# Kernel optimization log

Measured on AMD Instinct MI355X. Metric: run time of the kernel, lower is better.

Reference implementation:

```python
import jax, jax.numpy as jnp
import numpy as np

B, T, C = 4, 4096, 1024


def setup_inputs() -> dict:
    key = jax.random.key(0)
    k_x, k_f, k_g, k_p = jax.random.split(key, 4)
    scale = 1.0 / np.sqrt(C)  # keep gate pre-activations well-scaled
    return {
        "x": jax.random.normal(k_x, (B, T, C), dtype=jnp.float32),
        "W_f_x": jax.random.normal(k_f, (C, C), dtype=jnp.float32) * scale,
        "W_g_x": jax.random.normal(k_g, (C, C), dtype=jnp.float32) * scale,
        "W_proj": jax.random.normal(k_p, (C, C), dtype=jnp.float32) * scale,
    }


def _cfc_scan(a, b):
    """Solve h_t = a_t * h_{t-1} + b_t with h_{-1}=0 along axis 1 (T).

    Associative op on linear maps: (A_l,B_l) then (A_r,B_r) composes to
    (A_r*A_l, A_r*B_l + B_r). With h_init=0, h_t = B-component.
    """
    def op(l, r):
        al, bl = l
        ar, br = r
        return ar * al, ar * bl + br
    _, h = jax.lax.associative_scan(op, (a, b), axis=1)
    return h


def reference(x, W_f_x, W_g_x, W_proj):
    # Gates depend on x only (parallel mode). nn.Linear: x @ W.T
    f = jax.nn.sigmoid(jnp.einsum("btc,dc->btd", x, W_f_x))  # (B,T,C)
    g = jnp.tanh(jnp.einsum("btc,dc->btd", x, W_g_x))        # (B,T,C)
    h = _cfc_scan(f, (1.0 - f) * g)                           # (B,T,C)
    return jnp.einsum("btc,dc->btd", h, W_proj)               # c_proj
```

## Files before the change

kernel.cpp:

```cpp
#include <hip/hip_runtime.h>
#include <hip/hip_bf16.h>
#include <stdint.h>

#define TT 4096
#define BB 4
#define CC 1024
#define MM (BB * TT)
#define NCHUNK 64
#define CHUNK_T (TT / NCHUNK)
#define NCHAIN (BB * CC)

typedef float f32x4 __attribute__((ext_vector_type(4)));
typedef __bf16 bf16x8 __attribute__((ext_vector_type(8)));
typedef ushort us8 __attribute__((ext_vector_type(8)));

__device__ __forceinline__ float b2f(ushort u) {
  union { float f; uint32_t v; } x; x.v = ((uint32_t)u) << 16; return x.f;
}
__device__ __forceinline__ ushort f2b(float f) {
  union { float f; uint32_t u; } x; x.f = f;
  uint32_t r = x.u + 0x7fffu + ((x.u >> 16) & 1u);
  return (ushort)(r >> 16);
}

__device__ __forceinline__ void async_copy16(const ushort* g, ushort* l) {
  __builtin_amdgcn_global_load_lds(
      (__attribute__((address_space(1))) void*)(g),
      (__attribute__((address_space(3))) void*)(l), 16, 0, 0);
}

__global__ __launch_bounds__(256) void cvt_all(const float* __restrict__ x,
                                               const float* __restrict__ wf,
                                               const float* __restrict__ wg,
                                               const float* __restrict__ wp,
                                               ushort* __restrict__ xb,
                                               ushort* __restrict__ wcat,
                                               ushort* __restrict__ wpb) {
  const int i = blockIdx.x * 256 + threadIdx.x;
  const float* s; ushort* d; int off, dst;
  if (i < 4194304) {
    s = x; d = xb; off = i; dst = i;
  } else if (i < 4456448) {
    s = wf; d = wcat; off = i - 4194304;
    dst = ((off >> 8) << 9) + (off & 255);
  } else if (i < 4718592) {
    s = wg; d = wcat; off = i - 4456448;
    dst = ((off >> 8) << 9) + 256 + (off & 255);
  } else {
    s = wp; d = wpb; off = i - 4718592; dst = off;
  }
  float4 v = ((const float4*)s)[off];
  ushort4 o;
  o.x = f2b(v.x); o.y = f2b(v.y); o.z = f2b(v.z); o.w = f2b(v.w);
  ((ushort4*)d)[dst] = o;
}


#define RDA(sl, ih)                                                       \
  _Pragma("unroll") for (int i_ = 0; i_ < 4; ++i_)                        \
      af[i_] = *(const bf16x8*)(rA + (sl) * 8192 + (ih) * 2048 + i_ * 512);

#define RDB(sl)                                                           \
  _Pragma("unroll") for (int j_ = 0; j_ < 4; ++j_)                        \
      bfr[j_] = *(const bf16x8*)(rB + (sl) * 8192 + j_ * 512);

#define MFMA16(ih)                                                        \
  __builtin_amdgcn_s_setprio(1);                                          \
  _Pragma("unroll") for (int i_ = 0; i_ < 4; ++i_)                        \
  _Pragma("unroll") for (int j_ = 0; j_ < 4; ++j_)                        \
      acc[(ih) * 4 + i_][j_] = __builtin_amdgcn_mfma_f32_16x16x32_bf16(   \
          bfr[j_], af[i_], acc[(ih) * 4 + i_][j_], 0, 0, 0);              \
  __builtin_amdgcn_s_setprio(0)

#define MIDBAR()                                                          \
  __builtin_amdgcn_s_barrier();                                           \
  asm volatile("s_waitcnt lgkmcnt(0)" ::: "memory");                      \
  __builtin_amdgcn_sched_barrier(0)

#define ENDBAR()                                                          \
  __builtin_amdgcn_s_barrier();                                           \
  __builtin_amdgcn_sched_barrier(0)

#define CK4() asm volatile("s_waitcnt vmcnt(4)" ::: "memory")
#define CK0() asm volatile("s_waitcnt vmcnt(0)" ::: "memory")

#define TILE(S0, S1, NS0, NS1, KN)                                        \
  RDA(S0, 0); RDB(S0); stageA(NS0, (KN));      MIDBAR(); MFMA16(0);        ENDBAR(); \
  RDA(S0, 1);          stageB(NS0, (KN));      MIDBAR(); MFMA16(1); CK4(); ENDBAR(); \
  RDA(S1, 0); RDB(S1); stageA(NS1, (KN) + 32); MIDBAR(); MFMA16(0);        ENDBAR(); \
  RDA(S1, 1);          stageB(NS1, (KN) + 32); MIDBAR(); MFMA16(1); CK4(); ENDBAR();

template <int MODE>
__global__ __launch_bounds__(512, 2) void gemm_bt(const ushort* __restrict__ A,
                                                  const ushort* __restrict__ Bw,
                                                  float* __restrict__ outF,
                                                  ushort* __restrict__ outB,
                                                  float* __restrict__ cA2,
                                                  float* __restrict__ cB2, int N) {
  constexpr int K = CC;
  __shared__ __align__(16) ushort sA[4 * 256 * 32];
  __shared__ __align__(16) ushort sB[4 * 256 * 32];

  const int tid = threadIdx.x;
  const int lane = tid & 63;
  const int w = tid >> 6;
  const int wm = w >> 2;
  const int wn = w & 3;

  const int nbx = N >> 8;
  const int cpx = (int)gridDim.x >> 3;
  const int bid = blockIdx.x;
  const int wg = (bid & 7) * cpx + (bid >> 3);
  const long n0 = (long)(wg % nbx) << 8;
  const long m0 = (long)(wg / nbx) << 8;

  const int srow = lane >> 2;
  const int goct = (lane & 3) ^ ((lane >> 3) & 3);
  const ushort* gA0 = A + (m0 + w * 16 + srow) * K + goct * 8;
  const ushort* gB0 = Bw + (n0 + w * 16 + srow) * K + goct * 8;
  const ushort* gA1 = gA0 + 128 * (long)K;
  const ushort* gB1 = gB0 + 128 * (long)K;
  ushort* dA0 = &sA[w * 512 + lane * 8];
  ushort* dA1 = dA0 + 4096;
  ushort* dB0 = &sB[w * 512 + lane * 8];
  ushort* dB1 = dB0 + 4096;

  auto stageA = [&](int slot, int koff) {
    async_copy16(gA0 + koff, dA0 + slot * 8192);
    async_copy16(gA1 + koff, dA1 + slot * 8192);
  };
  auto stageB = [&](int slot, int koff) {
    async_copy16(gB0 + koff, dB0 + slot * 8192);
    async_copy16(gB1 + koff, dB1 + slot * 8192);
  };

  const int rlo = lane & 15;
  const int kq = lane >> 4;
  const int oslot = kq ^ ((rlo >> 1) & 3);
  const ushort* rA = &sA[(wm * 128 + rlo) * 32 + oslot * 8];
  const ushort* rB = &sB[(wn * 64 + rlo) * 32 + oslot * 8];

  f32x4 acc[8][4];
#pragma unroll
  for (int i = 0; i < 8; ++i)
#pragma unroll
    for (int j = 0; j < 4; ++j) acc[i][j] = (f32x4){0.f, 0.f, 0.f, 0.f};

  bf16x8 af[4], bfr[4];

  stageA(0, 0);
  stageB(0, 0);
  stageA(1, 32);
  stageB(1, 32);
  CK4();
  ENDBAR();

  for (int t2 = 0; t2 < 7; ++t2) {
    const int kn = t2 * 128 + 64;
    TILE(0, 1, 2, 3, kn);
    TILE(2, 3, 0, 1, kn + 64);
  }
  TILE(0, 1, 2, 3, 960);
  RDA(2, 0); RDB(2); MIDBAR(); MFMA16(0); ENDBAR();
  RDA(2, 1);         MIDBAR(); MFMA16(1); CK0(); ENDBAR();
  RDA(3, 0); RDB(3); MIDBAR(); MFMA16(0); ENDBAR();
  RDA(3, 1);         MIDBAR(); MFMA16(1);

  const int mloc = lane & 15;
  const int nq = (lane >> 4) * 4;

  if (MODE == 0) {
#pragma unroll
    for (int i = 0; i < 8; ++i) {
      const long m = m0 + wm * 128 + i * 16 + mloc;
#pragma unroll
      for (int j = 0; j < 4; ++j) {
        const long nb = n0 + wn * 64 + j * 16 + nq;
        *(f32x4*)(outF + m * N + nb) = acc[i][j];
      }
    }
  } else {
    const long bIdx = m0 >> 12;
    const int t0 = (int)(m0 & 4095) + wm * 128;
    const long chb = (n0 >> 1) + wn * 32;
    float* slab = (float*)((w < 4) ? &sA[w * 8192] : &sB[(w - 4) * 8192]);
    __builtin_amdgcn_s_barrier();
    __builtin_amdgcn_sched_barrier(0);

    const int chl = lane & 31;
    const int thf = lane >> 5;
#pragma unroll
    for (int rd = 0; rd < 2; ++rd) {
#pragma unroll
      for (int ii = 0; ii < 4; ++ii) {
        const int i = rd * 4 + ii;
        const long m = m0 + wm * 128 + i * 16 + mloc;
        const int tl = ii * 16 + mloc;
#pragma unroll
        for (int j = 0; j < 4; ++j) {
          const long nb = n0 + wn * 64 + j * 16 + nq;
          const f32x4 v = acc[i][j];
          float f0 = __builtin_amdgcn_rcpf(1.f + __expf(-v[0]));
          float g0 = fmaf(-2.f, __builtin_amdgcn_rcpf(1.f + __expf(2.f * v[1])), 1.f);
          float f1 = __builtin_amdgcn_rcpf(1.f + __expf(-v[2]));
          float g1 = fmaf(-2.f, __builtin_amdgcn_rcpf(1.f + __expf(2.f * v[3])), 1.f);
          ushort4 o;
          o.x = f2b(f0); o.y = f2b(g0); o.z = f2b(f1); o.w = f2b(g1);
          *(ushort4*)(outB + m * (long)N + nb) = o;
          const float fr0 = b2f(o.x), gr0 = b2f(o.y);
          const float fr1 = b2f(o.z), gr1 = b2f(o.w);
          const int c0 = j * 8 + (nq >> 1);
          float2 p0; p0.x = fr0; p0.y = (1.f - fr0) * gr0;
          float2 p1; p1.x = fr1; p1.y = (1.f - fr1) * gr1;
          *(float2*)(slab + (c0 * 64 + (tl ^ c0)) * 2) = p0;
          *(float2*)(slab + ((c0 + 1) * 64 + (tl ^ (c0 + 1))) * 2) = p1;
        }
      }
      asm volatile("s_waitcnt lgkmcnt(0)" ::: "memory");
      __builtin_amdgcn_sched_barrier(0);
      float Av = 1.f, Bv = 0.f;
#pragma unroll
      for (int s = 0; s < 32; ++s) {
        const int t = thf * 32 + s;
        const float2 ab = *(const float2*)(slab + (chl * 64 + (t ^ chl)) * 2);
        Bv = fmaf(ab.x, Bv, ab.y);
        Av *= ab.x;
      }
      const float Ao = __shfl_xor(Av, 32);
      const float Bo = __shfl_xor(Bv, 32);
      const float Af = (thf == 0) ? Ao * Av : Av * Ao;
      const float Bf = (thf == 0) ? fmaf(Ao, Bv, Bo) : fmaf(Av, Bo, Bv);
      if (thf == 0) {
        const int gchunk = (t0 >> 6) + rd;
        const long i0 = (bIdx * CC + chb + chl) * 64 + gchunk;
        cA2[i0] = Af;
        cB2[i0] = Bf;
      }
      if (rd == 0) {
        asm volatile("s_waitcnt lgkmcnt(0)" ::: "memory");
        __builtin_amdgcn_sched_barrier(0);
      }
    }
  }
}

__global__ __launch_bounds__(256) void scan_pass2(const float* __restrict__ cA2,
                                                  const float* __restrict__ cB2,
                                                  float* __restrict__ h2) {
  const int gid = blockIdx.x * 256 + threadIdx.x;
  const int chain = gid >> 6;
  const int lane = threadIdx.x & 63;
  float Av = cA2[chain * 64 + lane];
  float Bv = cB2[chain * 64 + lane];
#pragma unroll
  for (int m = 1; m < 64; m <<= 1) {
    const float Ao = __shfl_up(Av, m);
    const float Bo = __shfl_up(Bv, m);
    if (lane >= m) { Bv = fmaf(Av, Bo, Bv); Av = Av * Ao; }
  }
  const float Bx = __shfl_up(Bv, 1);
  h2[chain * 64 + lane] = (lane == 0) ? 0.f : Bx;
}

__global__ __launch_bounds__(256) void scan_pass3(const ushort* __restrict__ P,
                                                  const float* __restrict__ h2,
                                                  ushort* __restrict__ H) {
  const int pc = blockIdx.x * 256 + threadIdx.x;
  const int chunk = blockIdx.y;
  const int b = pc >> 9;
  const int c2 = (pc & 511) * 2;
  float h0 = h2[(b * CC + c2) * 64 + chunk];
  float h1 = h2[(b * CC + c2 + 1) * 64 + chunk];
  const ushort4* p =
      (const ushort4*)(P + (size_t)(b * TT + chunk * CHUNK_T) * (2 * CC) + c2 * 2);
  ushort2* hp = (ushort2*)(H + (size_t)(b * TT + chunk * CHUNK_T) * CC + c2);
#pragma unroll 8
  for (int i = 0; i < CHUNK_T; ++i) {
    const ushort4 v = p[0];
    p += 2 * CC / 4;
    const float f0 = b2f(v.x), g0 = b2f(v.y);
    const float f1 = b2f(v.z), g1 = b2f(v.w);
    h0 = fmaf(f0, h0, (1.f - f0) * g0);
    h1 = fmaf(f1, h1, (1.f - f1) * g1);
    ushort2 o;
    o.x = f2b(h0);
    o.y = f2b(h1);
    *hp = o;
    hp += CC / 2;
  }
}

extern "C" void kernel_launch(void* const* d_in, const int* in_sizes, int n_in,
                              void* d_out, int out_size, void* d_ws, size_t ws_size,
                              hipStream_t stream) {
  const float* x  = (const float*)d_in[0];
  const float* Wf = (const float*)d_in[1];
  const float* Wg = (const float*)d_in[2];
  const float* Wp = (const float*)d_in[3];

  char* ws = (char*)d_ws;
  ushort* xb   = (ushort*)(ws);
  ushort* Hb   = xb;
  ushort* Wcat = (ushort*)(ws + 33554432);
  ushort* Wpb  = (ushort*)(ws + 33554432 + 4194304);
  ushort* P    = (ushort*)(ws + 33554432 + 4194304 + 2097152);
  char* tail   = ws + 33554432 + 4194304 + 2097152 + 67108864;
  float* cA2   = (float*)(tail);
  float* cB2   = (float*)(tail + 1048576);
  float* h2    = (float*)(tail + 2097152);
  (void)ws_size; (void)in_sizes; (void)n_in; (void)out_size;

  cvt_all<<<19456, 256, 0, stream>>>(x, Wf, Wg, Wp, xb, Wcat, Wpb);

  gemm_bt<1><<<512, 512, 0, stream>>>(xb, Wcat, nullptr, P, cA2, cB2, 2 * CC);

  scan_pass2<<<NCHAIN * 64 / 256, 256, 0, stream>>>(cA2, cB2, h2);
  dim3 gs(NCHAIN / 2 / 256, NCHUNK);
  scan_pass3<<<gs, 256, 0, stream>>>(P, h2, Hb);

  gemm_bt<0><<<256, 512, 0, stream>>>(Hb, Wpb, (float*)d_out, nullptr, nullptr, nullptr, CC);
}
```

Measured before the change: 260.5 us.

## Fold chunk-prefix scan into pass3, relax GEMM barriers, unroll conversion kernel

Removes the separate scan_pass2 launch. Chunk carries are now stored chunk-major, and each scan_pass3 thread serially composes the preceding chunk summaries to get its starting state. The GEMM drops the sched_barrier on barriers that do not publish new LDS stages, which gives the compiler more freedom to schedule around them. The fp32-to-bf16 conversion kernel now does two elements per thread with half the grid. The cost is redundant serial prefix work in pass3 (up to 63 steps per thread for late chunks), which loads those blocks unevenly.

```diff
diff --git a/kernel.cpp b/kernel.cpp
--- a/kernel.cpp
+++ b/kernel.cpp
@@ -36,23 +36,27 @@
                                                ushort* __restrict__ xb,
                                                ushort* __restrict__ wcat,
                                                ushort* __restrict__ wpb) {
-  const int i = blockIdx.x * 256 + threadIdx.x;
-  const float* s; ushort* d; int off, dst;
-  if (i < 4194304) {
-    s = x; d = xb; off = i; dst = i;
-  } else if (i < 4456448) {
-    s = wf; d = wcat; off = i - 4194304;
-    dst = ((off >> 8) << 9) + (off & 255);
-  } else if (i < 4718592) {
-    s = wg; d = wcat; off = i - 4456448;
-    dst = ((off >> 8) << 9) + 256 + (off & 255);
-  } else {
-    s = wp; d = wpb; off = i - 4718592; dst = off;
-  }
-  float4 v = ((const float4*)s)[off];
-  ushort4 o;
-  o.x = f2b(v.x); o.y = f2b(v.y); o.z = f2b(v.z); o.w = f2b(v.w);
-  ((ushort4*)d)[dst] = o;
+  const int base = (blockIdx.x * 256 + threadIdx.x) * 2;
+#pragma unroll
+  for (int u = 0; u < 2; ++u) {
+    const int i = base + u;
+    const float* s; ushort* d; int off, dst;
+    if (i < 4194304) {
+      s = x; d = xb; off = i; dst = i;
+    } else if (i < 4456448) {
+      s = wf; d = wcat; off = i - 4194304;
+      dst = ((off >> 8) << 9) + (off & 255);
+    } else if (i < 4718592) {
+      s = wg; d = wcat; off = i - 4456448;
+      dst = ((off >> 8) << 9) + 256 + (off & 255);
+    } else {
+      s = wp; d = wpb; off = i - 4718592; dst = off;
+    }
+    float4 v = ((const float4*)s)[off];
+    ushort4 o;
+    o.x = f2b(v.x); o.y = f2b(v.y); o.z = f2b(v.z); o.w = f2b(v.w);
+    ((ushort4*)d)[dst] = o;
+  }
 }
 
 
@@ -77,7 +81,9 @@
   asm volatile("s_waitcnt lgkmcnt(0)" ::: "memory");                      \
   __builtin_amdgcn_sched_barrier(0)
 
-#define ENDBAR()                                                          \
+#define ENDBAR() __builtin_amdgcn_s_barrier()
+
+#define PUBBAR()                                                          \
   __builtin_amdgcn_s_barrier();                                           \
   __builtin_amdgcn_sched_barrier(0)
 
@@ -86,9 +92,9 @@
 
 #define TILE(S0, S1, NS0, NS1, KN)                                        \
   RDA(S0, 0); RDB(S0); stageA(NS0, (KN));      MIDBAR(); MFMA16(0);        ENDBAR(); \
-  RDA(S0, 1);          stageB(NS0, (KN));      MIDBAR(); MFMA16(1); CK4(); ENDBAR(); \
+  RDA(S0, 1);          stageB(NS0, (KN));      MIDBAR(); MFMA16(1); CK4(); PUBBAR(); \
   RDA(S1, 0); RDB(S1); stageA(NS1, (KN) + 32); MIDBAR(); MFMA16(0);        ENDBAR(); \
-  RDA(S1, 1);          stageB(NS1, (KN) + 32); MIDBAR(); MFMA16(1); CK4(); ENDBAR();
+  RDA(S1, 1);          stageB(NS1, (KN) + 32); MIDBAR(); MFMA16(1); CK4(); PUBBAR();
 
 template <int MODE>
 __global__ __launch_bounds__(512, 2) void gemm_bt(const ushort* __restrict__ A,
@@ -153,7 +159,7 @@
   stageA(1, 32);
   stageB(1, 32);
   CK4();
-  ENDBAR();
+  PUBBAR();
 
   for (int t2 = 0; t2 < 7; ++t2) {
     const int kn = t2 * 128 + 64;
@@ -162,7 +168,7 @@
   }
   TILE(0, 1, 2, 3, 960);
   RDA(2, 0); RDB(2); MIDBAR(); MFMA16(0); ENDBAR();
-  RDA(2, 1);         MIDBAR(); MFMA16(1); CK0(); ENDBAR();
+  RDA(2, 1);         MIDBAR(); MFMA16(1); CK0(); PUBBAR();
   RDA(3, 0); RDB(3); MIDBAR(); MFMA16(0); ENDBAR();
   RDA(3, 1);         MIDBAR(); MFMA16(1);
 
@@ -232,7 +238,7 @@
       const float Bf = (thf == 0) ? fmaf(Ao, Bv, Bo) : fmaf(Av, Bo, Bv);
       if (thf == 0) {
         const int gchunk = (t0 >> 6) + rd;
-        const long i0 = (bIdx * CC + chb + chl) * 64 + gchunk;
+        const long i0 = (long)gchunk * NCHAIN + (bIdx * CC + chb + chl);
         cA2[i0] = Af;
         cB2[i0] = Bf;
       }
@@ -244,33 +250,22 @@
   }
 }
 
-__global__ __launch_bounds__(256) void scan_pass2(const float* __restrict__ cA2,
+__global__ __launch_bounds__(256) void scan_pass3(const ushort* __restrict__ P,
+                                                  const float* __restrict__ cA2,
                                                   const float* __restrict__ cB2,
-                                                  float* __restrict__ h2) {
-  const int gid = blockIdx.x * 256 + threadIdx.x;
-  const int chain = gid >> 6;
-  const int lane = threadIdx.x & 63;
-  float Av = cA2[chain * 64 + lane];
-  float Bv = cB2[chain * 64 + lane];
-#pragma unroll
-  for (int m = 1; m < 64; m <<= 1) {
-    const float Ao = __shfl_up(Av, m);
-    const float Bo = __shfl_up(Bv, m);
-    if (lane >= m) { Bv = fmaf(Av, Bo, Bv); Av = Av * Ao; }
-  }
-  const float Bx = __shfl_up(Bv, 1);
-  h2[chain * 64 + lane] = (lane == 0) ? 0.f : Bx;
-}
-
-__global__ __launch_bounds__(256) void scan_pass3(const ushort* __restrict__ P,
-                                                  const float* __restrict__ h2,
                                                   ushort* __restrict__ H) {
   const int pc = blockIdx.x * 256 + threadIdx.x;
   const int chunk = blockIdx.y;
   const int b = pc >> 9;
   const int c2 = (pc & 511) * 2;
-  float h0 = h2[(b * CC + c2) * 64 + chunk];
-  float h1 = h2[(b * CC + c2 + 1) * 64 + chunk];
+  const int chain = b * CC + c2;
+  float h0 = 0.f, h1 = 0.f;
+  for (int j = 0; j < chunk; ++j) {
+    const float2 a  = *(const float2*)(cA2 + (size_t)j * NCHAIN + chain);
+    const float2 bb = *(const float2*)(cB2 + (size_t)j * NCHAIN + chain);
+    h0 = fmaf(a.x, h0, bb.x);
+    h1 = fmaf(a.y, h1, bb.y);
+  }
   const ushort4* p =
       (const ushort4*)(P + (size_t)(b * TT + chunk * CHUNK_T) * (2 * CC) + c2 * 2);
   ushort2* hp = (ushort2*)(H + (size_t)(b * TT + chunk * CHUNK_T) * CC + c2);
@@ -307,16 +302,14 @@
   char* tail   = ws + 33554432 + 4194304 + 2097152 + 67108864;
   float* cA2   = (float*)(tail);
   float* cB2   = (float*)(tail + 1048576);
-  float* h2    = (float*)(tail + 2097152);
   (void)ws_size; (void)in_sizes; (void)n_in; (void)out_size;
 
-  cvt_all<<<19456, 256, 0, stream>>>(x, Wf, Wg, Wp, xb, Wcat, Wpb);
+  cvt_all<<<9728, 256, 0, stream>>>(x, Wf, Wg, Wp, xb, Wcat, Wpb);
 
   gemm_bt<1><<<512, 512, 0, stream>>>(xb, Wcat, nullptr, P, cA2, cB2, 2 * CC);
 
-  scan_pass2<<<NCHAIN * 64 / 256, 256, 0, stream>>>(cA2, cB2, h2);
   dim3 gs(NCHAIN / 2 / 256, NCHUNK);
-  scan_pass3<<<gs, 256, 0, stream>>>(P, h2, Hb);
+  scan_pass3<<<gs, 256, 0, stream>>>(P, cA2, cB2, Hb);
 
   gemm_bt<0><<<256, 512, 0, stream>>>(Hb, Wpb, (float*)d_out, nullptr, nullptr, nullptr, CC);
 }
```

Measured after the change: 267.7 us. 1.03x slower.
